# Kernel optimization log

Hardware: AMD Instinct MI355X
Metric: run time of the kernel (lower is better)

Reference implementation:

```python
import jax, jax.numpy as jnp
import numpy as np

NUM_HEADS = 16
D_MODEL = 1024
HEAD_DIM = D_MODEL // NUM_HEADS
B, S = 2, 2048


def setup_inputs() -> dict:
    key = jax.random.key(0)
    ks = jax.random.split(key, 11)
    scale = 1.0 / np.sqrt(D_MODEL)
    inp = {
        'query': jax.random.normal(ks[0], (B, S, D_MODEL), jnp.float32),
        'key': jax.random.normal(ks[1], (B, S, D_MODEL), jnp.float32),
        'value': jax.random.normal(ks[2], (B, S, D_MODEL), jnp.float32),
        'Wq': jax.random.normal(ks[3], (D_MODEL, D_MODEL), jnp.float32) * scale,
        'bq': jnp.zeros((D_MODEL,), jnp.float32),
        'Wk': jax.random.normal(ks[4], (D_MODEL, D_MODEL), jnp.float32) * scale,
        'bk': jnp.zeros((D_MODEL,), jnp.float32),
        'Wv': jax.random.normal(ks[5], (D_MODEL, D_MODEL), jnp.float32) * scale,
        'bv': jnp.zeros((D_MODEL,), jnp.float32),
        'Wo': jax.random.normal(ks[6], (D_MODEL, D_MODEL), jnp.float32) * scale,
        'bo': jnp.zeros((D_MODEL,), jnp.float32),
    }
    return inp


def reference(query, key, value, Wq, bq, Wk, bk, Wv, bv, Wo, bo):
    b, s, _ = query.shape
    # Linear projections (torch Linear: x @ W.T + b; here W stored as [in,out])
    Q = query @ Wq + bq
    K = key @ Wk + bk
    V = value @ Wv + bv
    # [B, H, S, Dh]
    Q = Q.reshape(b, s, NUM_HEADS, HEAD_DIM).transpose(0, 2, 1, 3)
    K = K.reshape(b, -1, NUM_HEADS, HEAD_DIM).transpose(0, 2, 1, 3)
    V = V.reshape(b, -1, NUM_HEADS, HEAD_DIM).transpose(0, 2, 1, 3)
    scores = jnp.einsum('bhqd,bhkd->bhqk', Q, K) / jnp.sqrt(jnp.float32(HEAD_DIM)).astype(Q.dtype)
    attn = jax.nn.softmax(scores, axis=-1)
    ctx = jnp.einsum('bhqk,bhkd->bhqd', attn, V)
    ctx = ctx.transpose(0, 2, 1, 3).reshape(b, s, D_MODEL)
    return ctx @ Wo + bo
```

## Files before the change

kernel.cpp:

```cpp
#include <hip/hip_runtime.h>
#include <hip/hip_bf16.h>
#include <math.h>

#define NUM_HEADS 16
#define D_MODEL 1024
#define HEAD_DIM 64
#define BATCH 2
#define SEQ 2048
#define M_TOTAL (BATCH*SEQ)

typedef __bf16 bf16;
typedef __bf16 bf16x2 __attribute__((ext_vector_type(2)));
typedef __bf16 bf16x4 __attribute__((ext_vector_type(4)));
typedef __bf16 bf16x8 __attribute__((ext_vector_type(8)));
typedef float  floatx4  __attribute__((ext_vector_type(4)));
typedef float  floatx16 __attribute__((ext_vector_type(16)));
typedef unsigned int uintx4 __attribute__((ext_vector_type(4)));

#define CLSCALE 0.180336884f

#if __has_builtin(__builtin_amdgcn_exp2f)
#define EXP2(x) __builtin_amdgcn_exp2f(x)
#else
#define EXP2(x) exp2f(x)
#endif

__device__ __forceinline__ void async_copy16(const bf16* g, bf16* l) {
    __builtin_amdgcn_global_load_lds(
        (const __attribute__((address_space(1))) void*)g,
        (__attribute__((address_space(3))) void*)l, 16, 0, 0);
}

__device__ __forceinline__ unsigned pk2(float lo, float hi) {
    bf16x2 t; t[0] = (bf16)lo; t[1] = (bf16)hi;
    return __builtin_bit_cast(unsigned, t);
}

__global__ __launch_bounds__(256)
void convert_kernel(const float* __restrict__ Wq, const float* __restrict__ Wk,
                    const float* __restrict__ Wv, const float* __restrict__ Wo,
                    const float* __restrict__ q, const float* __restrict__ k,
                    const float* __restrict__ v,
                    bf16* __restrict__ Wt, bf16* __restrict__ Xb)
{
    const int blk = blockIdx.x;
    const int tid = threadIdx.x;
    if (blk < 256) {
        const int wi  = blk >> 6;
        const int sub = blk & 63;
        const int xb  = sub & 3;
        const int yb  = sub >> 2;
        const float* W = (wi == 0) ? Wq : (wi == 1) ? Wk : (wi == 2) ? Wv : Wo;
        bf16* dstM = Wt + (size_t)wi * D_MODEL * D_MODEL;
        const int n  = xb * 256 + tid;
        const int k0 = yb * 64;
        bf16* dst = dstM + (size_t)n * D_MODEL + k0;
        #pragma unroll
        for (int jc = 0; jc < 8; ++jc) {
            bf16x8 w;
            #pragma unroll
            for (int j = 0; j < 8; ++j)
                w[j] = (bf16)W[(size_t)(k0 + jc * 8 + j) * D_MODEL + n];
            *(bf16x8*)(dst + jc * 8) = w;
        }
    } else {
        const int rem   = blk - 256;
        const int plane = rem >> 11;
        const int xb    = rem & 2047;
        const float* X = (plane == 0) ? q : (plane == 1) ? k : v;
        bf16* dst = Xb + (size_t)plane * M_TOTAL * D_MODEL;
        size_t i = ((size_t)xb * 256 + tid) * 8;
        const float4 u = *(const float4*)(X + i);
        const float4 w = *(const float4*)(X + i + 4);
        bf16x8 o;
        o[0] = (bf16)u.x; o[1] = (bf16)u.y; o[2] = (bf16)u.z; o[3] = (bf16)u.w;
        o[4] = (bf16)w.x; o[5] = (bf16)w.y; o[6] = (bf16)w.z; o[7] = (bf16)w.w;
        *(bf16x8*)(dst + i) = o;
    }
}

__global__ __launch_bounds__(256)
void proj_kernel(const bf16* __restrict__ Xb, const bf16* __restrict__ Wt,
                 const float* __restrict__ bq, const float* __restrict__ bk,
                 const float* __restrict__ bv,
                 bf16* __restrict__ Qo, bf16* __restrict__ Ko, bf16* __restrict__ Vto)
{
    const int lin  = blockIdx.x;
    const int xcd  = lin & 7;
    const int idx  = lin >> 3;
    const int nt   = idx & 7;
    const int t2   = idx >> 3;
    const int mloc = t2 & 3;
    const int which= t2 >> 2;
    const int tileM = (xcd * 4 + mloc) * 128;
    const int tileN = nt * 128;

    const bf16* X     = Xb + (size_t)which * M_TOTAL * D_MODEL;
    const bf16* Wm    = Wt + (size_t)which * D_MODEL * D_MODEL;
    const float* bias = (which == 0) ? bq : (which == 1) ? bk : bv;

    const int tid  = threadIdx.x;
    const int lane = tid & 63;
    const int wave = tid >> 6;
    const int quad = lane >> 4;
    const int l16  = lane & 15;

    __shared__ bf16 sA[128 * 32];
    __shared__ bf16 sB[128 * 32];

    floatx4 acc[4][4];
    const floatx4 z4 = {0.0f, 0.0f, 0.0f, 0.0f};
    #pragma unroll
    for (int i = 0; i < 4; i++)
        #pragma unroll
        for (int j = 0; j < 4; j++) acc[i][j] = z4;

    const int wm = (wave >> 1) * 64;
    const int wn = (wave & 1) * 64;

    const int c0   = wave * 64 + lane;
    const int row0 = c0 >> 2, col0 = ((c0 & 3) ^ ((row0 >> 1) & 3)) * 8;
    const int c1   = c0 + 256;
    const int row1 = c1 >> 2, col1 = ((c1 & 3) ^ ((row1 >> 1) & 3)) * 8;
    bf16* ldsA0 = sA + (size_t)(wave * 64) * 8;
    bf16* ldsA1 = sA + (size_t)(256 + wave * 64) * 8;
    bf16* ldsB0 = sB + (size_t)(wave * 64) * 8;
    bf16* ldsB1 = sB + (size_t)(256 + wave * 64) * 8;

    for (int k0 = 0; k0 < D_MODEL; k0 += 32) {
        __syncthreads();
        async_copy16(X  + (size_t)(tileM + row0) * D_MODEL + k0 + col0, ldsA0);
        async_copy16(X  + (size_t)(tileM + row1) * D_MODEL + k0 + col1, ldsA1);
        async_copy16(Wm + (size_t)(tileN + row0) * D_MODEL + k0 + col0, ldsB0);
        async_copy16(Wm + (size_t)(tileN + row1) * D_MODEL + k0 + col1, ldsB1);
        __syncthreads();

        bf16x8 af[4], bfr[4];
        #pragma unroll
        for (int i = 0; i < 4; i++) {
            const int RA = wm + i * 16 + l16;
            const int jA = quad ^ ((RA >> 1) & 3);
            af[i]  = *(const bf16x8*)&sA[RA * 32 + jA * 8];
        }
        #pragma unroll
        for (int j = 0; j < 4; j++) {
            const int RB = wn + j * 16 + l16;
            const int jB = quad ^ ((RB >> 1) & 3);
            bfr[j] = *(const bf16x8*)&sB[RB * 32 + jB * 8];
        }
        if (which != 2) {
            #pragma unroll
            for (int i = 0; i < 4; i++)
                #pragma unroll
                for (int j = 0; j < 4; j++)
                    acc[i][j] = __builtin_amdgcn_mfma_f32_16x16x32_bf16(af[i], bfr[j], acc[i][j], 0, 0, 0);
        } else {
            #pragma unroll
            for (int i = 0; i < 4; i++)
                #pragma unroll
                for (int j = 0; j < 4; j++)
                    acc[i][j] = __builtin_amdgcn_mfma_f32_16x16x32_bf16(bfr[i], af[j], acc[i][j], 0, 0, 0);
        }
    }

    if (which != 2) {
        bf16* out = (which == 0) ? Qo : Ko;
        const float oscale = (which == 0) ? CLSCALE : 1.0f;
        #pragma unroll
        for (int i = 0; i < 4; i++) {
            int mbase = tileM + wm + i * 16 + quad * 4;
            #pragma unroll
            for (int j = 0; j < 4; j++) {
                int n = tileN + wn + j * 16 + l16;
                float bb = bias[n];
                int h = n >> 6, d = n & 63;
                #pragma unroll
                for (int r = 0; r < 4; r++) {
                    int mm = mbase + r;
                    int b = mm >> 11, s = mm & 2047;
                    out[(((size_t)(b * NUM_HEADS + h)) * SEQ + s) * HEAD_DIM + d] =
                        (bf16)((acc[i][j][r] + bb) * oscale);
                }
            }
        }
    } else {
        #pragma unroll
        for (int i = 0; i < 4; i++) {
            #pragma unroll
            for (int r = 0; r < 4; r++) {
                int n = tileN + wn + i * 16 + quad * 4 + r;
                float bb = bias[n];
                int h = n >> 6, d = n & 63;
                #pragma unroll
                for (int j = 0; j < 4; j++) {
                    int m = tileM + wm + j * 16 + l16;
                    int b = m >> 11, s = m & 2047;
                    Vto[(((size_t)(b * NUM_HEADS + h)) * HEAD_DIM + d) * SEQ + s] =
                        (bf16)(acc[i][j][r] + bb);
                }
            }
        }
    }
}

__global__ __launch_bounds__(512)
void attn_kernel(const bf16* __restrict__ Q, const bf16* __restrict__ K,
                 const bf16* __restrict__ Vt, bf16* __restrict__ Ctx)
{
    const int lin    = blockIdx.x;
    const int xcd    = lin & 7;
    const int rest   = lin >> 3;
    const int superg = rest >> 4;
    const int qi     = rest & 15;
    const int bh     = superg * 8 + xcd;
    const int b      = bh >> 4, h = bh & 15;
    const int q0     = qi * 128;

    const int tid  = threadIdx.x;
    const int lane = tid & 63;
    const int wave = tid >> 6;
    const int half = lane >> 5;
    const int m31  = lane & 31;
    const int xs   = m31 & 7;

    const int qsub  = wave & 3;
    const int kjsub = wave >> 2;

    __shared__ bf16 sK[2][64 * 64];
    __shared__ bf16 sV[2][64 * 64];
    __shared__ float sL[128];

    const bf16* Qb  = Q  + ((size_t)bh * SEQ + q0) * HEAD_DIM;
    const bf16* Kb  = K  + (size_t)bh * SEQ * HEAD_DIM;
    const bf16* Vtb = Vt + (size_t)bh * HEAD_DIM * SEQ;

    bf16x8 bQ[4];
    #pragma unroll
    for (int s = 0; s < 4; s++)
        bQ[s] = *(const bf16x8*)(Qb + (size_t)(qsub * 32 + m31) * HEAD_DIM + s * 16 + half * 8);

    bf16x8 vONE;
    #pragma unroll
    for (int j = 0; j < 8; j++) vONE[j] = (bf16)1.0f;

    {
        const int c    = tid;
        const int row  = c >> 3;
        const int scol = ((c & 7) ^ (row & 7)) * 8;
        async_copy16(Kb  + (size_t)row * HEAD_DIM + scol, &sK[0][c * 8]);
        async_copy16(Vtb + (size_t)row * SEQ + scol,      &sV[0][c * 8]);
    }

    floatx16 o0, o1;
    floatx16 lacc;
    #pragma unroll
    for (int r = 0; r < 16; r++) { o0[r] = 0.0f; o1[r] = 0.0f; lacc[r] = 0.0f; }

    for (int kt = 0; kt < SEQ / 64; ++kt) {
        const int p = kt & 1;
        __syncthreads();

        bf16x8 aK[4];
        #pragma unroll
        for (int s = 0; s < 4; s++)
            aK[s] = *(const bf16x8*)&sK[p][(kjsub * 32 + m31) * 64 + (((2 * s + half) ^ xs) * 8)];

        if (kt + 1 < SEQ / 64) {
            const int c    = tid;
            const int row  = c >> 3;
            const int scol = ((c & 7) ^ (row & 7)) * 8;
            async_copy16(Kb  + (size_t)((kt + 1) * 64 + row) * HEAD_DIM + scol,
                         &sK[p ^ 1][c * 8]);
            async_copy16(Vtb + (size_t)row * SEQ + (kt + 1) * 64 + scol,
                         &sV[p ^ 1][c * 8]);
        }

        floatx16 sc;
        #pragma unroll
        for (int r = 0; r < 16; r++) sc[r] = 0.0f;
        __builtin_amdgcn_s_setprio(1);
        #pragma unroll
        for (int s = 0; s < 4; s++)
            sc = __builtin_amdgcn_mfma_f32_32x32x16_bf16(aK[s], bQ[s], sc, 0, 0, 0);
        __builtin_amdgcn_s_setprio(0);

        #pragma unroll
        for (int r = 0; r < 16; r++) sc[r] = EXP2(sc[r]);

        bf16x8 bP[2];
        #pragma unroll
        for (int s = 0; s < 2; s++) {
            const int bs = 8 * s;
            unsigned x = pk2(sc[bs + 0], sc[bs + 1]);
            unsigned z = pk2(sc[bs + 2], sc[bs + 3]);
            unsigned y = pk2(sc[bs + 4], sc[bs + 5]);
            unsigned w = pk2(sc[bs + 6], sc[bs + 7]);
            auto r0 = __builtin_amdgcn_permlane32_swap(x, y, false, false);
            auto r1 = __builtin_amdgcn_permlane32_swap(z, w, false, false);
            uintx4 bp;
            bp[0] = r0[0]; bp[1] = r1[0]; bp[2] = r0[1]; bp[3] = r1[1];
            bP[s] = __builtin_bit_cast(bf16x8, bp);
        }

        __builtin_amdgcn_s_setprio(1);
        #pragma unroll
        for (int s = 0; s < 2; s++) {
            int ch = ((4 * kjsub + 2 * s + half) ^ xs) * 8;
            bf16x8 a0 = *(const bf16x8*)&sV[p][(size_t)m31 * 64 + ch];
            bf16x8 a1 = *(const bf16x8*)&sV[p][(size_t)(32 + m31) * 64 + ch];
            o0 = __builtin_amdgcn_mfma_f32_32x32x16_bf16(a0, bP[s], o0, 0, 0, 0);
            o1 = __builtin_amdgcn_mfma_f32_32x32x16_bf16(a1, bP[s], o1, 0, 0, 0);
            lacc = __builtin_amdgcn_mfma_f32_32x32x16_bf16(vONE, bP[s], lacc, 0, 0, 0);
        }
        __builtin_amdgcn_s_setprio(0);
    }

    float lp = lacc[0];

    __syncthreads();
    float* fO = (qsub == 0) ? (float*)&sK[0][0] :
                (qsub == 1) ? (float*)&sK[1][0] :
                (qsub == 2) ? (float*)&sV[0][0] : (float*)&sV[1][0];
    if (kjsub == 1) {
        #pragma unroll
        for (int r = 0; r < 16; r++) {
            fO[r * 64 + lane]        = o0[r];
            fO[1024 + r * 64 + lane] = o1[r];
        }
        if (half == 0) sL[qsub * 32 + m31] = lp;
    }
    __syncthreads();
    if (kjsub == 0) {
        #pragma unroll
        for (int r = 0; r < 16; r++) {
            o0[r] += fO[r * 64 + lane];
            o1[r] += fO[1024 + r * 64 + lane];
        }
        float denom = lp + sL[qsub * 32 + m31];
        float inv = 1.0f / denom;

        int q = q0 + qsub * 32 + m31;
        size_t base = ((size_t)b * SEQ + q) * D_MODEL + h * HEAD_DIM;
        #pragma unroll
        for (int rg = 0; rg < 4; rg++) {
            int d0 = rg * 8 + half * 4;
            bf16x4 w0, w1;
            #pragma unroll
            for (int i = 0; i < 4; i++) {
                w0[i] = (bf16)(o0[rg * 4 + i] * inv);
                w1[i] = (bf16)(o1[rg * 4 + i] * inv);
            }
            *(bf16x4*)&Ctx[base + d0]      = w0;
            *(bf16x4*)&Ctx[base + 32 + d0] = w1;
        }
    }
}

__global__ __launch_bounds__(256)
void out_proj_kernel(const bf16* __restrict__ A, const bf16* __restrict__ Wto,
                     const float* __restrict__ bias, float* __restrict__ Out)
{
    const int lin  = blockIdx.x;
    const int xcd  = lin & 7;
    const int idx  = lin >> 3;
    const int nt   = idx & 15;
    const int mloc = idx >> 4;
    const int tileM = (xcd * 4 + mloc) * 128;
    const int tileN = nt * 64;

    const int tid  = threadIdx.x;
    const int lane = tid & 63;
    const int wave = tid >> 6;
    const int quad = lane >> 4;
    const int l16  = lane & 15;

    __shared__ bf16 sA[128 * 32];
    __shared__ bf16 sB[64 * 32];

    floatx4 acc[4][2];
    const floatx4 z4 = {0.0f, 0.0f, 0.0f, 0.0f};
    #pragma unroll
    for (int i = 0; i < 4; i++)
        #pragma unroll
        for (int j = 0; j < 2; j++) acc[i][j] = z4;

    const int wm = (wave >> 1) * 64;
    const int wn = (wave & 1) * 32;

    const int c0   = wave * 64 + lane;
    const int row0 = c0 >> 2, col0 = ((c0 & 3) ^ ((row0 >> 1) & 3)) * 8;
    const int c1   = c0 + 256;
    const int row1 = c1 >> 2, col1 = ((c1 & 3) ^ ((row1 >> 1) & 3)) * 8;
    bf16* ldsA0 = sA + (size_t)(wave * 64) * 8;
    bf16* ldsA1 = sA + (size_t)(256 + wave * 64) * 8;
    bf16* ldsB0 = sB + (size_t)(wave * 64) * 8;

    for (int k0 = 0; k0 < D_MODEL; k0 += 32) {
        __syncthreads();
        async_copy16(A   + (size_t)(tileM + row0) * D_MODEL + k0 + col0, ldsA0);
        async_copy16(A   + (size_t)(tileM + row1) * D_MODEL + k0 + col1, ldsA1);
        async_copy16(Wto + (size_t)(tileN + row0) * D_MODEL + k0 + col0, ldsB0);
        __syncthreads();

        bf16x8 af[4], bfr[2];
        #pragma unroll
        for (int i = 0; i < 4; i++) {
            const int RA = wm + i * 16 + l16;
            const int jA = quad ^ ((RA >> 1) & 3);
            af[i]  = *(const bf16x8*)&sA[RA * 32 + jA * 8];
        }
        #pragma unroll
        for (int j = 0; j < 2; j++) {
            const int RB = wn + j * 16 + l16;
            const int jB = quad ^ ((RB >> 1) & 3);
            bfr[j] = *(const bf16x8*)&sB[RB * 32 + jB * 8];
        }

        #pragma unroll
        for (int i = 0; i < 4; i++)
            #pragma unroll
            for (int j = 0; j < 2; j++)
                acc[i][j] = __builtin_amdgcn_mfma_f32_16x16x32_bf16(af[i], bfr[j], acc[i][j], 0, 0, 0);
    }

    #pragma unroll
    for (int i = 0; i < 4; i++) {
        int mbase = tileM + wm + i * 16 + quad * 4;
        #pragma unroll
        for (int j = 0; j < 2; j++) {
            int n = tileN + wn + j * 16 + l16;
            float bb = bias[n];
            #pragma unroll
            for (int r = 0; r < 4; r++)
                Out[(size_t)(mbase + r) * D_MODEL + n] = acc[i][j][r] + bb;
        }
    }
}

extern "C" void kernel_launch(void* const* d_in, const int* in_sizes, int n_in,
                              void* d_out, int out_size, void* d_ws, size_t ws_size,
                              hipStream_t stream)
{
    const float* q  = (const float*)d_in[0];
    const float* k  = (const float*)d_in[1];
    const float* v  = (const float*)d_in[2];
    const float* Wq = (const float*)d_in[3];
    const float* bq = (const float*)d_in[4];
    const float* Wk = (const float*)d_in[5];
    const float* bk = (const float*)d_in[6];
    const float* Wv = (const float*)d_in[7];
    const float* bv = (const float*)d_in[8];
    const float* Wo = (const float*)d_in[9];
    const float* bo = (const float*)d_in[10];
    float* out = (float*)d_out;

    const size_t PLANE = (size_t)M_TOTAL * D_MODEL;
    bf16* Qb = (bf16*)d_ws;
    bf16* Kb = Qb + PLANE;
    bf16* Vt = Kb + PLANE;
    bf16* Cb = Vt + PLANE;
    bf16* Wt = Cb + PLANE;
    bf16* Xb = Wt + 4 * (size_t)D_MODEL * D_MODEL;

    convert_kernel<<<dim3(6400), 256, 0, stream>>>(Wq, Wk, Wv, Wo, q, k, v, Wt, Xb);
    proj_kernel<<<dim3(768), 256, 0, stream>>>(Xb, Wt, bq, bk, bv, Qb, Kb, Vt);
    attn_kernel<<<dim3(512), 512, 0, stream>>>(Qb, Kb, Vt, Cb);
    out_proj_kernel<<<dim3(512), 256, 0, stream>>>(Cb, Wt + 3 * (size_t)D_MODEL * D_MODEL, bo, out);
}
```

Measured before the change: 226.2 us.

## Double-buffer LDS tiles in QKV and output projection GEMMs

Both projection GEMMs now use two LDS buffers per operand. The next K-slice is issued with async copies right after the current fragments are read into registers, so the global loads overlap the MFMA work, and one barrier per iteration replaces two. This doubles LDS use per block, which may lower occupancy. It also relies on the async copy having landed by the following barrier.

Result: no change. 222.7 us, median of 3 (-1.6%).

```diff
diff --git a/kernel.cpp b/kernel.cpp
--- a/kernel.cpp
+++ b/kernel.cpp
@@ -105,8 +105,8 @@
     const int quad = lane >> 4;
     const int l16  = lane & 15;
 
-    __shared__ bf16 sA[128 * 32];
-    __shared__ bf16 sB[128 * 32];
+    __shared__ bf16 sA[2][4096];
+    __shared__ bf16 sB[2][4096];
 
     floatx4 acc[4][4];
     const floatx4 z4 = {0.0f, 0.0f, 0.0f, 0.0f};
@@ -122,17 +122,20 @@
     const int row0 = c0 >> 2, col0 = ((c0 & 3) ^ ((row0 >> 1) & 3)) * 8;
     const int c1   = c0 + 256;
     const int row1 = c1 >> 2, col1 = ((c1 & 3) ^ ((row1 >> 1) & 3)) * 8;
-    bf16* ldsA0 = sA + (size_t)(wave * 64) * 8;
-    bf16* ldsA1 = sA + (size_t)(256 + wave * 64) * 8;
-    bf16* ldsB0 = sB + (size_t)(wave * 64) * 8;
-    bf16* ldsB1 = sB + (size_t)(256 + wave * 64) * 8;
-
-    for (int k0 = 0; k0 < D_MODEL; k0 += 32) {
-        __syncthreads();
-        async_copy16(X  + (size_t)(tileM + row0) * D_MODEL + k0 + col0, ldsA0);
-        async_copy16(X  + (size_t)(tileM + row1) * D_MODEL + k0 + col1, ldsA1);
-        async_copy16(Wm + (size_t)(tileN + row0) * D_MODEL + k0 + col0, ldsB0);
-        async_copy16(Wm + (size_t)(tileN + row1) * D_MODEL + k0 + col1, ldsB1);
+    const int dA0 = wave * 64 * 8;
+    const int dA1 = (256 + wave * 64) * 8;
+
+    auto stage = [&](int buf, int k0) {
+        async_copy16(X  + (size_t)(tileM + row0) * D_MODEL + k0 + col0, &sA[buf][dA0]);
+        async_copy16(X  + (size_t)(tileM + row1) * D_MODEL + k0 + col1, &sA[buf][dA1]);
+        async_copy16(Wm + (size_t)(tileN + row0) * D_MODEL + k0 + col0, &sB[buf][dA0]);
+        async_copy16(Wm + (size_t)(tileN + row1) * D_MODEL + k0 + col1, &sB[buf][dA1]);
+    };
+
+    stage(0, 0);
+
+    for (int kt = 0; kt < 32; ++kt) {
+        const int p = kt & 1;
         __syncthreads();
 
         bf16x8 af[4], bfr[4];
@@ -140,14 +143,17 @@
         for (int i = 0; i < 4; i++) {
             const int RA = wm + i * 16 + l16;
             const int jA = quad ^ ((RA >> 1) & 3);
-            af[i]  = *(const bf16x8*)&sA[RA * 32 + jA * 8];
+            af[i]  = *(const bf16x8*)&sA[p][RA * 32 + jA * 8];
         }
         #pragma unroll
         for (int j = 0; j < 4; j++) {
             const int RB = wn + j * 16 + l16;
             const int jB = quad ^ ((RB >> 1) & 3);
-            bfr[j] = *(const bf16x8*)&sB[RB * 32 + jB * 8];
-        }
+            bfr[j] = *(const bf16x8*)&sB[p][RB * 32 + jB * 8];
+        }
+
+        if (kt < 31) stage(p ^ 1, (kt + 1) * 32);
+
         if (which != 2) {
             #pragma unroll
             for (int i = 0; i < 4; i++)
@@ -374,8 +380,8 @@
     const int quad = lane >> 4;
     const int l16  = lane & 15;
 
-    __shared__ bf16 sA[128 * 32];
-    __shared__ bf16 sB[64 * 32];
+    __shared__ bf16 sA[2][4096];
+    __shared__ bf16 sB[2][2048];
 
     floatx4 acc[4][2];
     const floatx4 z4 = {0.0f, 0.0f, 0.0f, 0.0f};
@@ -391,15 +397,19 @@
     const int row0 = c0 >> 2, col0 = ((c0 & 3) ^ ((row0 >> 1) & 3)) * 8;
     const int c1   = c0 + 256;
     const int row1 = c1 >> 2, col1 = ((c1 & 3) ^ ((row1 >> 1) & 3)) * 8;
-    bf16* ldsA0 = sA + (size_t)(wave * 64) * 8;
-    bf16* ldsA1 = sA + (size_t)(256 + wave * 64) * 8;
-    bf16* ldsB0 = sB + (size_t)(wave * 64) * 8;
-
-    for (int k0 = 0; k0 < D_MODEL; k0 += 32) {
-        __syncthreads();
-        async_copy16(A   + (size_t)(tileM + row0) * D_MODEL + k0 + col0, ldsA0);
-        async_copy16(A   + (size_t)(tileM + row1) * D_MODEL + k0 + col1, ldsA1);
-        async_copy16(Wto + (size_t)(tileN + row0) * D_MODEL + k0 + col0, ldsB0);
+    const int dA0 = wave * 64 * 8;
+    const int dA1 = (256 + wave * 64) * 8;
+
+    auto stage = [&](int buf, int k0) {
+        async_copy16(A   + (size_t)(tileM + row0) * D_MODEL + k0 + col0, &sA[buf][dA0]);
+        async_copy16(A   + (size_t)(tileM + row1) * D_MODEL + k0 + col1, &sA[buf][dA1]);
+        async_copy16(Wto + (size_t)(tileN + row0) * D_MODEL + k0 + col0, &sB[buf][dA0]);
+    };
+
+    stage(0, 0);
+
+    for (int kt = 0; kt < 32; ++kt) {
+        const int p = kt & 1;
         __syncthreads();
 
         bf16x8 af[4], bfr[2];
@@ -407,14 +417,16 @@
         for (int i = 0; i < 4; i++) {
             const int RA = wm + i * 16 + l16;
             const int jA = quad ^ ((RA >> 1) & 3);
-            af[i]  = *(const bf16x8*)&sA[RA * 32 + jA * 8];
+            af[i]  = *(const bf16x8*)&sA[p][RA * 32 + jA * 8];
         }
         #pragma unroll
         for (int j = 0; j < 2; j++) {
             const int RB = wn + j * 16 + l16;
             const int jB = quad ^ ((RB >> 1) & 3);
-            bfr[j] = *(const bf16x8*)&sB[RB * 32 + jB * 8];
-        }
+            bfr[j] = *(const bf16x8*)&sB[p][RB * 32 + jB * 8];
+        }
+
+        if (kt < 31) stage(p ^ 1, (kt + 1) * 32);
 
         #pragma unroll
         for (int i = 0; i < 4; i++)
```
